# Kernel optimization log

Measured on AMD Instinct MI355X. Metric: run time of the kernel, lower is better.

Reference implementation:

```python
import jax, jax.numpy as jnp
import numpy as np

RF = 3          # receptive_field_size (cubic)
STRIDE = 1
TEMP = 1.0      # softmax temperature ('soft' sampling, eval mode: no Gumbel noise)
TREE_DEPTH = 4

# Truth table of all 16 binary gates: GATES[g, t] = value of gate g on input
# pattern t = 2*a + b (a = first child, b = second child), t in {0,1,2,3}.
GATES = np.array([[(g >> t) & 1 for t in range(4)] for g in range(16)],
                 dtype=np.float32)  # (16, 4)


def _lut_eval(a, b, w):
    """Differentiable 2-input LUT. a, b: (B,K,P,nodes); w: (nodes,K,16)."""
    probs = jax.nn.softmax(w / TEMP, axis=-1)          # (nodes,K,16)
    lut = probs @ jnp.asarray(GATES)                   # (nodes,K,4) relaxed truth table
    lut = jnp.moveaxis(lut, 0, 1)[:, None]             # (K,1,nodes,4) -> bcast over B,P
    l0, l1, l2, l3 = lut[..., 0], lut[..., 1], lut[..., 2], lut[..., 3]
    na, nb = 1.0 - a, 1.0 - b
    # E[lut(a,b)] under independent Bernoulli inputs
    return l0 * na * nb + l1 * na * b + l2 * a * nb + l3 * a * b


def setup_inputs() -> dict:
    key = jax.random.key(0)
    ks = jax.random.split(key, 8)
    B, C, H, W, D = 4, 3, 32, 32, 32
    K, S = 32, 16  # num_kernels, lut_rank**tree_depth leaves
    x = jax.random.uniform(ks[0], (B, C, H, W, D), dtype=jnp.float32)
    # (lut_rank=2, K, S, 4) coords (h, w, d, c); rf=3 and channels=3 so all in [0,3)
    kernel_coords = jax.random.randint(ks[1], (2, K, S, 4), 0, 3, dtype=jnp.int32)
    w0 = jax.random.normal(ks[2], (16, K, 16), dtype=jnp.float32)
    w1 = jax.random.normal(ks[3], (8, K, 16), dtype=jnp.float32)
    w2 = jax.random.normal(ks[4], (4, K, 16), dtype=jnp.float32)
    w3 = jax.random.normal(ks[5], (2, K, 16), dtype=jnp.float32)
    w4 = jax.random.normal(ks[6], (1, K, 16), dtype=jnp.float32)
    return {"x": x, "kernel_coords": kernel_coords,
            "w0": w0, "w1": w1, "w2": w2, "w3": w3, "w4": w4}


def reference(x, kernel_coords, w0, w1, w2, w3, w4):
    B, C, H, W, D = x.shape
    OH, OW, OD = (H - RF) // STRIDE + 1, (W - RF) // STRIDE + 1, (D - RF) // STRIDE + 1
    kc = kernel_coords
    # linear offset of each leaf coord inside flattened (C,H,W,D) volume
    base = ((kc[..., 3] * H + kc[..., 0]) * W + kc[..., 1]) * D + kc[..., 2]  # (2,K,S)
    oh = jnp.arange(OH) * STRIDE
    ow = jnp.arange(OW) * STRIDE
    od = jnp.arange(OD) * STRIDE
    patch = ((oh[:, None, None] * W + ow[None, :, None]) * D
             + od[None, None, :]).reshape(-1)                                  # (P,)
    lin = base[:, :, None, :] + patch[None, None, :, None]                     # (2,K,P,S)
    g = x.reshape(B, -1)[:, lin]                                               # (B,2,K,P,S)
    out = _lut_eval(g[:, 0], g[:, 1], w0)                                      # (B,K,P,S)
    for w in (w1, w2, w3, w4):  # binary tree reduction over TREE_DEPTH levels
        out = _lut_eval(out[..., 0::2], out[..., 1::2], w)
    return out.reshape(B, out.shape[1], OH, OW, OD)
```

## Files before the change

kernel.cpp:

```cpp
#include <hip/hip_runtime.h>


#define B_  4
#define C_  3
#define H_  32
#define W_  32
#define D_  32
#define K_  32
#define S_  16
#define TPB 256

typedef float v8f __attribute__((ext_vector_type(8), aligned(4)));

__device__ __forceinline__ v8f lut8(v8f a, v8f b, float l0, float d1, float d2, float d3) {
    v8f t = a * d2 + l0;
    t = b * d1 + t;
    t = (a * b) * d3 + t;
    return t;
}

__global__ __launch_bounds__(TPB, 3) void logic_conv3d(
    const float* __restrict__ x,
    const int*   __restrict__ kc,
    const float* __restrict__ w0,
    const float* __restrict__ w1,
    const float* __restrict__ w2,
    const float* __restrict__ w3,
    const float* __restrict__ w4,
    float*       __restrict__ out)
{
    __shared__ float4 s_lut[31];
    __shared__ int    s_lb[32];

    const int bk  = blockIdx.x;
    const int b   = bk >> 5;
    const int k   = bk & 31;
    const int tid = threadIdx.x;

    if (tid < 31) {
        const float* wp; int ln;
        if      (tid < 16) { wp = w0; ln = tid;      }
        else if (tid < 24) { wp = w1; ln = tid - 16; }
        else if (tid < 28) { wp = w2; ln = tid - 24; }
        else if (tid < 30) { wp = w3; ln = tid - 28; }
        else               { wp = w4; ln = 0;        }
        const float* wrow = wp + (ln * K_ + k) * 16;
        float lg[16];
        float m = -1e30f;
        #pragma unroll
        for (int g = 0; g < 16; ++g) { lg[g] = wrow[g]; m = fmaxf(m, lg[g]); }
        float z = 0.f;
        #pragma unroll
        for (int g = 0; g < 16; ++g) { lg[g] = __expf(lg[g] - m); z += lg[g]; }
        const float inv = 1.0f / z;
        float l0 = 0.f, l1 = 0.f, l2 = 0.f, l3 = 0.f;
        #pragma unroll
        for (int g = 0; g < 16; ++g) {
            float p = lg[g] * inv;
            if (g & 1) l0 += p;
            if (g & 2) l1 += p;
            if (g & 4) l2 += p;
            if (g & 8) l3 += p;
        }
        s_lut[tid] = make_float4(l0, l1 - l0, l2 - l0, (l3 - l2) - (l1 - l0));
    } else if (tid >= 32 && tid < 64) {
        const int idx  = tid - 32;
        const int tree = idx >> 4;
        const int s    = idx & 15;
        const int off  = ((tree * K_ + k) * S_ + s) * 4;
        const int h = kc[off + 0], w = kc[off + 1], d = kc[off + 2], c = kc[off + 3];
        s_lb[idx] = ((c * H_ + h) * W_ + w) * D_ + d;
    }
    __syncthreads();

    int sA[16], sB[16];
    #pragma unroll
    for (int s = 0; s < 16; ++s) {
        sA[s] = __builtin_amdgcn_readfirstlane(s_lb[s]);
        sB[s] = __builtin_amdgcn_readfirstlane(s_lb[16 + s]);
    }

    const int g   = tid & 3;
    const int woi = tid >> 2;
    const int ohl = woi >> 5;
    int ow        = woi & 31;
    if (ow > 29) ow = 29;
    const int od0 = (g < 3) ? (g << 3) : 22;
    const int oh  = blockIdx.y * 2 + ohl;
    const int vo  = ohl * (W_ * D_) + ow * D_ + od0;

    const float* xb2 = x + (size_t)b * (C_ * H_ * W_ * D_) + (blockIdx.y * 2) * (W_ * D_);

    v8f v1[8];
    #pragma unroll
    for (int j = 0; j < 8; ++j) {
        const int s0 = 2 * j, s1 = 2 * j + 1;
        const v8f A0 = *(const v8f*)(xb2 + sA[s0] + vo);
        const v8f B0 = *(const v8f*)(xb2 + sB[s0] + vo);
        const float4 L0 = s_lut[s0];
        const v8f t0 = lut8(A0, B0, L0.x, L0.y, L0.z, L0.w);
        const v8f A1 = *(const v8f*)(xb2 + sA[s1] + vo);
        const v8f B1 = *(const v8f*)(xb2 + sB[s1] + vo);
        const float4 L1 = s_lut[s1];
        const v8f t1 = lut8(A1, B1, L1.x, L1.y, L1.z, L1.w);
        const float4 LN = s_lut[16 + j];
        v1[j] = lut8(t0, t1, LN.x, LN.y, LN.z, LN.w);
    }

    #pragma unroll
    for (int j = 0; j < 4; ++j) {
        const float4 L = s_lut[24 + j];
        v1[j] = lut8(v1[2 * j], v1[2 * j + 1], L.x, L.y, L.z, L.w);
    }
    #pragma unroll
    for (int j = 0; j < 2; ++j) {
        const float4 L = s_lut[28 + j];
        v1[j] = lut8(v1[2 * j], v1[2 * j + 1], L.x, L.y, L.z, L.w);
    }
    {
        const float4 L = s_lut[30];
        v1[0] = lut8(v1[0], v1[1], L.x, L.y, L.z, L.w);
    }

    float* outp = out + (size_t)bk * 27000 + oh * 900 + ow * 30 + od0;
    *(v8f*)outp = v1[0];
}

extern "C" void kernel_launch(void* const* d_in, const int* in_sizes, int n_in,
                              void* d_out, int out_size, void* d_ws, size_t ws_size,
                              hipStream_t stream) {
    const float* x  = (const float*)d_in[0];
    const int*   kc = (const int*)d_in[1];
    const float* w0 = (const float*)d_in[2];
    const float* w1 = (const float*)d_in[3];
    const float* w2 = (const float*)d_in[4];
    const float* w3 = (const float*)d_in[5];
    const float* w4 = (const float*)d_in[6];
    float* out = (float*)d_out;

    dim3 grid(B_ * K_, 15);
    logic_conv3d<<<grid, TPB, 0, stream>>>(x, kc, w0, w1, w2, w3, w4, out);
}
```

Before: 89.81 us.

## Stage input slab in LDS with padded stride and factor LUT arithmetic

Each block cooperatively loads the 3-channel by 4-row input slab into shared memory with a padded row stride, then runs all 32 leaf gathers from LDS instead of global/L1. This removes repeated global gathers of the same neighbourhood across leaves. The LUT evaluation is also refactored to use two FMAs plus one instead of a separate multiply. The cost is about 50KB of LDS per block, which may cut occupancy below the launch-bounds target, plus an extra barrier and unaligned LDS vector reads.

Result: faster. 87.49 us (-2.6%).

```diff
diff --git a/kernel.cpp b/kernel.cpp
--- a/kernel.cpp
+++ b/kernel.cpp
@@ -8,15 +8,15 @@
 #define D_  32
 #define K_  32
 #define S_  16
+#define WS  33
 #define TPB 256
 
 typedef float v8f __attribute__((ext_vector_type(8), aligned(4)));
 
 __device__ __forceinline__ v8f lut8(v8f a, v8f b, float l0, float d1, float d2, float d3) {
-    v8f t = a * d2 + l0;
-    t = b * d1 + t;
-    t = (a * b) * d3 + t;
-    return t;
+    const v8f t0 = a * d2 + l0;
+    const v8f t1 = a * d3 + d1;
+    return b * t1 + t0;
 }
 
 __global__ __launch_bounds__(TPB, 3) void logic_conv3d(
@@ -31,6 +31,7 @@
 {
     __shared__ float4 s_lut[31];
     __shared__ int    s_lb[32];
+    __shared__ __align__(16) float slab[12 * 32 * WS];
 
     const int bk  = blockIdx.x;
     const int b   = bk >> 5;
@@ -69,61 +70,77 @@
         const int s    = idx & 15;
         const int off  = ((tree * K_ + k) * S_ + s) * 4;
         const int h = kc[off + 0], w = kc[off + 1], d = kc[off + 2], c = kc[off + 3];
-        s_lb[idx] = ((c * H_ + h) * W_ + w) * D_ + d;
+        s_lb[idx] = ((c * 4 + h) * 32 + w) * WS + d;
+    }
+
+    {
+        const float* xb = x + (size_t)b * (C_ * H_ * W_ * D_) + (blockIdx.y * 2) * (W_ * D_);
+        const int w  = tid >> 3;
+        const int d4 = (tid & 7) << 2;
+        #pragma unroll
+        for (int it = 0; it < 12; ++it) {
+            const int c  = it >> 2;
+            const int dh = it & 3;
+            const float4 val = *(const float4*)(xb + c * (H_ * W_ * D_) + dh * (W_ * D_) + tid * 4);
+            *(float4*)&slab[((c * 4 + dh) * 32 + w) * WS + d4] = val;
+        }
     }
     __syncthreads();
 
-    int sA[16], sB[16];
+    int sAB[32];
     #pragma unroll
-    for (int s = 0; s < 16; ++s) {
-        sA[s] = __builtin_amdgcn_readfirstlane(s_lb[s]);
-        sB[s] = __builtin_amdgcn_readfirstlane(s_lb[16 + s]);
+    for (int i = 0; i < 8; ++i) {
+        const int4 q = *(const int4*)&s_lb[i * 4];
+        sAB[i * 4 + 0] = __builtin_amdgcn_readfirstlane(q.x);
+        sAB[i * 4 + 1] = __builtin_amdgcn_readfirstlane(q.y);
+        sAB[i * 4 + 2] = __builtin_amdgcn_readfirstlane(q.z);
+        sAB[i * 4 + 3] = __builtin_amdgcn_readfirstlane(q.w);
     }
 
-    const int g   = tid & 3;
-    const int woi = tid >> 2;
-    const int ohl = woi >> 5;
-    int ow        = woi & 31;
-    if (ow > 29) ow = 29;
-    const int od0 = (g < 3) ? (g << 3) : 22;
-    const int oh  = blockIdx.y * 2 + ohl;
-    const int vo  = ohl * (W_ * D_) + ow * D_ + od0;
+    const int ohl = tid >> 7;
+    const int r   = tid & 127;
+    const int ow  = r >> 2;
+    const int gq  = r & 3;
+    const int od0 = (gq < 3) ? (gq << 3) : 22;
 
-    const float* xb2 = x + (size_t)b * (C_ * H_ * W_ * D_) + (blockIdx.y * 2) * (W_ * D_);
+    if (ow < 30) {
+        const int vo = ohl * (32 * WS) + ow * WS + od0;
 
-    v8f v1[8];
-    #pragma unroll
-    for (int j = 0; j < 8; ++j) {
-        const int s0 = 2 * j, s1 = 2 * j + 1;
-        const v8f A0 = *(const v8f*)(xb2 + sA[s0] + vo);
-        const v8f B0 = *(const v8f*)(xb2 + sB[s0] + vo);
-        const float4 L0 = s_lut[s0];
-        const v8f t0 = lut8(A0, B0, L0.x, L0.y, L0.z, L0.w);
-        const v8f A1 = *(const v8f*)(xb2 + sA[s1] + vo);
-        const v8f B1 = *(const v8f*)(xb2 + sB[s1] + vo);
-        const float4 L1 = s_lut[s1];
-        const v8f t1 = lut8(A1, B1, L1.x, L1.y, L1.z, L1.w);
-        const float4 LN = s_lut[16 + j];
-        v1[j] = lut8(t0, t1, LN.x, LN.y, LN.z, LN.w);
+        v8f v1[8];
+        #pragma unroll
+        for (int j = 0; j < 8; ++j) {
+            const int s0 = 2 * j, s1 = 2 * j + 1;
+            const v8f A0 = *(const v8f*)&slab[sAB[s0] + vo];
+            const v8f B0 = *(const v8f*)&slab[sAB[16 + s0] + vo];
+            const float4 L0 = s_lut[s0];
+            const v8f t0 = lut8(A0, B0, L0.x, L0.y, L0.z, L0.w);
+            const v8f A1 = *(const v8f*)&slab[sAB[s1] + vo];
+            const v8f B1 = *(const v8f*)&slab[sAB[16 + s1] + vo];
+            const float4 L1 = s_lut[s1];
+            const v8f t1 = lut8(A1, B1, L1.x, L1.y, L1.z, L1.w);
+            const float4 LN = s_lut[16 + j];
+            v1[j] = lut8(t0, t1, LN.x, LN.y, LN.z, LN.w);
+        }
+
+        #pragma unroll
+        for (int j = 0; j < 4; ++j) {
+            const float4 L = s_lut[24 + j];
+            v1[j] = lut8(v1[2 * j], v1[2 * j + 1], L.x, L.y, L.z, L.w);
+        }
+        #pragma unroll
+        for (int j = 0; j < 2; ++j) {
+            const float4 L = s_lut[28 + j];
+            v1[j] = lut8(v1[2 * j], v1[2 * j + 1], L.x, L.y, L.z, L.w);
+        }
+        {
+            const float4 L = s_lut[30];
+            v1[0] = lut8(v1[0], v1[1], L.x, L.y, L.z, L.w);
+        }
+
+        const int oh = blockIdx.y * 2 + ohl;
+        float* outp = out + (size_t)bk * 27000 + oh * 900 + ow * 30 + od0;
+        *(v8f*)outp = v1[0];
     }
-
-    #pragma unroll
-    for (int j = 0; j < 4; ++j) {
-        const float4 L = s_lut[24 + j];
-        v1[j] = lut8(v1[2 * j], v1[2 * j + 1], L.x, L.y, L.z, L.w);
-    }
-    #pragma unroll
-    for (int j = 0; j < 2; ++j) {
-        const float4 L = s_lut[28 + j];
-        v1[j] = lut8(v1[2 * j], v1[2 * j + 1], L.x, L.y, L.z, L.w);
-    }
-    {
-        const float4 L = s_lut[30];
-        v1[0] = lut8(v1[0], v1[1], L.x, L.y, L.z, L.w);
-    }
-
-    float* outp = out + (size_t)bk * 27000 + oh * 900 + ow * 30 + od0;
-    *(v8f*)outp = v1[0];
 }
 
 extern "C" void kernel_launch(void* const* d_in, const int* in_sizes, int n_in,
```
